# Performance work log

Hardware: AMD Instinct MI355X
Metric: run time of the kernel (lower is better)

Reference implementation:

```python
import jax, jax.numpy as jnp
import numpy as np

B, TV, TL = 4, 13600, 256
VD, LD, E, H = 256, 768, 256, 8
HD = E // H
SCALE = HD ** -0.5
CLAMP = 50000.0
NEG = -9e15


def _xavier(k, out_d, in_d):
    lim = np.sqrt(6.0 / (in_d + out_d)).astype(np.float32)
    return jax.random.uniform(k, (out_d, in_d), minval=-lim, maxval=lim, dtype=jnp.float32)


def setup_inputs() -> dict:
    key = jax.random.key(0)
    ks = jax.random.split(key, 10)
    return {
        "v": jax.random.normal(ks[0], (B, TV, VD), dtype=jnp.float32),
        "l": jax.random.normal(ks[1], (B, TL, LD), dtype=jnp.float32),
        "v_pos": jax.random.normal(ks[2], (B, TV, VD), dtype=jnp.float32),
        "attention_mask_v": jnp.ones((B, TV), dtype=jnp.float32),
        "attention_mask_l": jnp.ones((B, TL), dtype=jnp.float32),
        "Wq": _xavier(ks[3], E, VD), "bq": jnp.zeros((E,), jnp.float32),
        "Wk": _xavier(ks[4], E, LD), "bk": jnp.zeros((E,), jnp.float32),
        "Wvv": _xavier(ks[5], E, VD), "bvv": jnp.zeros((E,), jnp.float32),
        "Wvl": _xavier(ks[6], E, LD), "bvl": jnp.zeros((E,), jnp.float32),
        "Wov": _xavier(ks[7], VD, E), "bov": jnp.zeros((VD,), jnp.float32),
        "Wol": _xavier(ks[8], LD, E), "bol": jnp.zeros((LD,), jnp.float32),
    }


def _heads(x):  # [B, T, E] -> [B, H, T, HD]
    b, t, _ = x.shape
    return x.reshape(b, t, H, HD).transpose(0, 2, 1, 3)


def reference(v, l, v_pos, attention_mask_v, attention_mask_l,
              Wq, bq, Wk, bk, Wvv, bvv, Wvl, bvl, Wov, bov, Wol, bol):
    # projections (eval mode: dropout disabled)
    q = _heads(((v + v_pos) @ Wq.T + bq) * SCALE)        # [B,H,TV,HD]
    k = _heads(l @ Wk.T + bk)                             # [B,H,TL,HD]
    val_v = _heads(v @ Wvv.T + bvv)                       # [B,H,TV,HD]
    val_l = _heads(l @ Wvl.T + bvl)                       # [B,H,TL,HD]

    # shared scores, computed once: [B,H,TV,TL]
    aw = jnp.einsum('bhtd,bhsd->bhts', q, k)
    aw = jnp.clip(aw, -CLAMP, CLAMP)

    # language-direction scores: transpose, stabilize, clamp
    aw_l = aw.transpose(0, 1, 3, 2)                       # [B,H,TL,TV]
    aw_l = aw_l - jnp.max(aw_l, axis=-1, keepdims=True)
    aw_l = jnp.clip(aw_l, -CLAMP, CLAMP)
    # torch masked_fill(mask==0, NEG) then + : nonzero mask values are ADDED
    mv = jnp.where(attention_mask_v == 0, NEG, attention_mask_v)[:, None, None, :]
    aw_l = aw_l + mv
    p_l = jax.nn.softmax(aw_l, axis=-1)

    # vision-direction scores
    ml = jnp.where(attention_mask_l == 0, NEG, attention_mask_l)[:, None, None, :]
    p_v = jax.nn.softmax(aw + ml, axis=-1)

    out_v = jnp.einsum('bhts,bhsd->bhtd', p_v, val_l)     # [B,H,TV,HD]
    out_l = jnp.einsum('bhst,bhtd->bhsd', p_l, val_v)     # [B,H,TL,HD]
    out_v = out_v.transpose(0, 2, 1, 3).reshape(B, TV, E) @ Wov.T + bov
    out_l = out_l.transpose(0, 2, 1, 3).reshape(B, TL, E) @ Wol.T + bol
    return (out_v, out_l)
```

## Files before the change

kernel.cpp:

```cpp
#include <hip/hip_runtime.h>
#include <math.h>


typedef unsigned short u16;
typedef unsigned int   u32;
typedef __attribute__((ext_vector_type(4))) u16 us4;
typedef __attribute__((ext_vector_type(8))) u16 us8;
typedef __attribute__((ext_vector_type(8))) short s8b;
typedef __attribute__((ext_vector_type(4))) float f4;

#define B_   4
#define TV_  13600
#define TL_  256
#define VD_  256
#define LD_  768
#define E_   256
#define H_   8
#define HD_  32
#define PREC 36

static constexpr float SCALE_  = 0.17677669529663687f;
static constexpr float CLAMP_  = 50000.0f;
static constexpr float NEG_    = -9e15f;
static constexpr float LOG2E_  = 1.4426950408889634f;

__device__ __forceinline__ float bf2f(u16 x) {
    return __uint_as_float(((u32)x) << 16);
}
__device__ __forceinline__ u16 f2bf(float f) {
    u32 u = __float_as_uint(f);
    u += 0x7fffu + ((u >> 16) & 1u);
    return (u16)(u >> 16);
}

__device__ __forceinline__ s8b frag32(const u16* base, int row, int q) {
    int slot = q ^ ((row >> 1) & 3);
    return *(const s8b*)(base + row * 32 + slot * 8);
}

__global__ void sniff_kernel(const void* __restrict__ mask, int* __restrict__ flag) {
    if (threadIdx.x == 0 && blockIdx.x == 0) {
        u32 w = *(const u32*)mask;
        *flag = (w == 0x3F800000u) ? 1 : 0;
    }
}

__global__ __launch_bounds__(256) void prep_v_kernel(
    const int* __restrict__ flag, const void* __restrict__ v,
    const void* __restrict__ vp, u16* __restrict__ vb, u16* __restrict__ vqb)
{
    const bool f32 = (*flag != 0);
    const size_t n = (size_t)B_ * TV_ * VD_;
    size_t i = ((size_t)blockIdx.x * 256 + threadIdx.x) * 4;
    const size_t stride = (size_t)gridDim.x * 256 * 4;
    for (; i < n; i += stride) {
        float a[4], b[4];
        if (f32) {
            float4 x = ((const float4*)v)[i >> 2];
            float4 y = ((const float4*)vp)[i >> 2];
            a[0]=x.x; a[1]=x.y; a[2]=x.z; a[3]=x.w;
            b[0]=y.x; b[1]=y.y; b[2]=y.z; b[3]=y.w;
        } else {
            us4 x = ((const us4*)v)[i >> 2];
            us4 y = ((const us4*)vp)[i >> 2];
            #pragma unroll
            for (int j = 0; j < 4; ++j) { a[j]=bf2f(x[j]); b[j]=bf2f(y[j]); }
        }
        us4 o1, o2;
        #pragma unroll
        for (int j = 0; j < 4; ++j) { o1[j]=f2bf(a[j]); o2[j]=f2bf(a[j]+b[j]); }
        ((us4*)vb)[i >> 2] = o1;
        ((us4*)vqb)[i >> 2] = o2;
    }
}

struct Seg { const void* src; void* dst; int n; int toF32; };
struct PrepArgs { Seg s[13]; };

__global__ __launch_bounds__(256) void prep_rest_kernel(
    const int* __restrict__ flag, PrepArgs args)
{
    const bool f32 = (*flag != 0);
    for (int k = 0; k < 13; ++k) {
        Seg sg = args.s[k];
        for (int j = blockIdx.x * 256 + threadIdx.x; j < sg.n;
             j += gridDim.x * 256) {
            float x = f32 ? ((const float*)sg.src)[j] : bf2f(((const u16*)sg.src)[j]);
            if (sg.toF32) ((float*)sg.dst)[j] = x;
            else          ((u16*)sg.dst)[j]   = f2bf(x);
        }
    }
}

template<bool CEXT>
__global__ __launch_bounds__(256) void gemm_mfma(
    const int* __restrict__ flag,
    const u16* __restrict__ A, const u16* __restrict__ W,
    const float* __restrict__ bias, void* __restrict__ C, size_t c_off,
    int N, int K, float scale)
{
    __shared__ __align__(16) u16 As[128 * 32];
    __shared__ __align__(16) u16 Bs[128 * 32];
    const int tid  = threadIdx.x;
    const int lane = tid & 63, wid = tid >> 6;
    const int wm = wid >> 1, wn = wid & 1;
    const size_t m0 = (size_t)blockIdx.x * 128;
    const int n0 = blockIdx.y * 128;

    const int srow = tid >> 1;
    const int half = tid & 1;
    const int ssw  = (srow >> 1) & 3;
    const int sl0  = half * 2, sl1 = half * 2 + 1;

    f4 acc[4][4];
    #pragma unroll
    for (int i = 0; i < 4; ++i)
        #pragma unroll
        for (int j = 0; j < 4; ++j) acc[i][j] = (f4){0.f, 0.f, 0.f, 0.f};

    for (int k0 = 0; k0 < K; k0 += 32) {
        {
            const u16* ga = A + (m0 + srow) * (size_t)K + k0;
            *(us8*)&As[srow*32 + sl0*8] = *(const us8*)(ga + (sl0 ^ ssw) * 8);
            *(us8*)&As[srow*32 + sl1*8] = *(const us8*)(ga + (sl1 ^ ssw) * 8);
            const u16* gb = W + ((size_t)(n0 + srow)) * (size_t)K + k0;
            *(us8*)&Bs[srow*32 + sl0*8] = *(const us8*)(gb + (sl0 ^ ssw) * 8);
            *(us8*)&Bs[srow*32 + sl1*8] = *(const us8*)(gb + (sl1 ^ ssw) * 8);
        }
        __syncthreads();
        s8b af[4], bf[4];
        const int q = lane >> 4;
        #pragma unroll
        for (int mt = 0; mt < 4; ++mt)
            af[mt] = frag32(As, wm*64 + mt*16 + (lane & 15), q);
        #pragma unroll
        for (int nt = 0; nt < 4; ++nt)
            bf[nt] = frag32(Bs, wn*64 + nt*16 + (lane & 15), q);
        #pragma unroll
        for (int mt = 0; mt < 4; ++mt)
            #pragma unroll
            for (int nt = 0; nt < 4; ++nt)
                acc[mt][nt] = __builtin_amdgcn_mfma_f32_16x16x32_bf16(
                    af[mt], bf[nt], acc[mt][nt], 0, 0, 0);
        __syncthreads();
    }

    const int q = lane >> 4;
    const bool f32out = CEXT ? (*flag != 0) : false;
    #pragma unroll
    for (int nt = 0; nt < 4; ++nt) {
        const int col = n0 + wn*64 + nt*16 + (lane & 15);
        const float bv = bias[col];
        #pragma unroll
        for (int mt = 0; mt < 4; ++mt) {
            #pragma unroll
            for (int reg = 0; reg < 4; ++reg) {
                const size_t row = m0 + wm*64 + mt*16 + q*4 + reg;
                const float val = (acc[mt][nt][reg] + bv) * scale;
                const size_t idx = c_off + row * (size_t)N + col;
                if (CEXT && f32out) ((float*)C)[idx] = val;
                else                ((u16*)C)[idx]   = f2bf(val);
            }
        }
    }
}

__global__ __launch_bounds__(256, 4) void attn_v_mfma(
    const int* __restrict__ flag,
    const u16* __restrict__ qm, const u16* __restrict__ km,
    const u16* __restrict__ vm, const void* __restrict__ maskl,
    u16* __restrict__ outm)
{
    __shared__ __align__(16) u16 Qs[64 * 32];
    __shared__ __align__(16) u16 Ks[256 * 32];
    __shared__ __align__(16) u16 VTs[32 * 264];
    __shared__ float mls[256];

    const int tid = threadIdx.x, lane = tid & 63, wid = tid >> 6;
    const int bb = blockIdx.z, hh = blockIdx.y;
    const int t0 = blockIdx.x * 64;
    const int q  = lane >> 4;
    const int l15 = lane & 15;

    {
        int row = tid >> 2, slot = tid & 3;
        int sw = (row >> 1) & 3;
        int tg = t0 + row; if (tg >= TV_) tg = TV_ - 1;
        const u16* gp = qm + ((size_t)(bb*TV_ + tg)) * E_ + hh*HD_;
        *(us8*)&Qs[row*32 + slot*8] = *(const us8*)(gp + ((slot ^ sw) * 8));
    }
    {
        int s = tid, sw = (s >> 1) & 3;
        const u16* gp = km + ((size_t)(bb*TL_ + s)) * E_ + hh*HD_;
        #pragma unroll
        for (int slot = 0; slot < 4; ++slot)
            *(us8*)&Ks[s*32 + slot*8] = *(const us8*)(gp + ((slot ^ sw) * 8));
    }
    {
        int s = tid;
        const u16* gp = vm + ((size_t)(bb*TL_ + s)) * E_ + hh*HD_;
        #pragma unroll
        for (int d0 = 0; d0 < 32; d0 += 8) {
            us8 vv = *(const us8*)(gp + d0);
            #pragma unroll
            for (int j = 0; j < 8; ++j) VTs[(d0 + j)*264 + s] = vv[j];
        }
        float mv = (*flag) ? ((const float*)maskl)[(size_t)bb*TL_ + s]
                           : bf2f(((const u16*)maskl)[(size_t)bb*TL_ + s]);
        mls[s] = (mv == 0.0f) ? NEG_ : mv;
    }
    __syncthreads();

    const s8b qf = frag32(Qs, wid*16 + l15, q);
    f4 sacc[16];
    #pragma unroll
    for (int mt = 0; mt < 16; ++mt) {
        s8b kf = frag32(Ks, mt*16 + l15, q);
        f4 z = {0.f, 0.f, 0.f, 0.f};
        sacc[mt] = __builtin_amdgcn_mfma_f32_16x16x32_bf16(kf, qf, z, 0, 0, 0);
    }

    float vmax = -1e30f;
    #pragma unroll
    for (int mt = 0; mt < 16; ++mt) {
        f4 mv4 = *(const f4*)&mls[mt*16 + q*4];
        #pragma unroll
        for (int r = 0; r < 4; ++r) {
            float v = fminf(fmaxf(sacc[mt][r], -CLAMP_), CLAMP_) + mv4[r];
            sacc[mt][r] = v;
            vmax = fmaxf(vmax, v);
        }
    }
    vmax = fmaxf(vmax, __shfl_xor(vmax, 16));
    vmax = fmaxf(vmax, __shfl_xor(vmax, 32));

    float sum = 0.f;
    us4 pws[16];
    #pragma unroll
    for (int mt = 0; mt < 16; ++mt) {
        #pragma unroll
        for (int r = 0; r < 4; ++r) {
            float p = exp2f((sacc[mt][r] - vmax) * LOG2E_);
            u16 pb = f2bf(p);
            pws[mt][r] = pb;
            sum += bf2f(pb);
        }
    }
    sum += __shfl_xor(sum, 16);
    sum += __shfl_xor(sum, 32);
    float Lreg[4];
    #pragma unroll
    for (int r = 0; r < 4; ++r) Lreg[r] = __shfl(sum, q*4 + r);

    __syncthreads();

    u16* myP = Ks + wid * (16 * 40);
    f4 oacc[2];
    oacc[0] = (f4){0.f,0.f,0.f,0.f};
    oacc[1] = (f4){0.f,0.f,0.f,0.f};
    #pragma unroll
    for (int ks = 0; ks < 8; ++ks) {
        *(us4*)&myP[l15*40 + q*4]      = pws[2*ks];
        *(us4*)&myP[l15*40 + 16 + q*4] = pws[2*ks + 1];
        s8b pa = *(const s8b*)&myP[l15*40 + q*8];
        #pragma unroll
        for (int nt = 0; nt < 2; ++nt) {
            s8b vb = *(const s8b*)&VTs[(nt*16 + l15)*264 + ks*32 + q*8];
            oacc[nt] = __builtin_amdgcn_mfma_f32_16x16x32_bf16(pa, vb, oacc[nt], 0, 0, 0);
        }
    }

    #pragma unroll
    for (int r = 0; r < 4; ++r) {
        const int tg = t0 + wid*16 + q*4 + r;
        if (tg < TV_) {
            const float inv = 1.0f / Lreg[r];
            #pragma unroll
            for (int nt = 0; nt < 2; ++nt)
                outm[((size_t)(bb*TV_ + tg)) * E_ + hh*HD_ + nt*16 + l15] =
                    f2bf(oacc[nt][r] * inv);
        }
    }
}

__global__ __launch_bounds__(256, 6) void attn_l_mfma(
    const int* __restrict__ flag,
    const u16* __restrict__ qm, const u16* __restrict__ km,
    const u16* __restrict__ vm, const void* __restrict__ maskv,
    u16* __restrict__ part, int nchunk, int chunk)
{
    __shared__ __align__(16) u16 smem0[128 * 40];
    __shared__ __align__(16) u16 Qs[32 * 32];
    __shared__ __align__(16) u16 VTs[32 * 32];
    __shared__ float mvs[32];

    const int tid = threadIdx.x, lane = tid & 63, wid = tid >> 6;
    const int bb = blockIdx.z, hh = blockIdx.y;
    const int tc  = blockIdx.x >> 1;
    const int s0b = (blockIdx.x & 1) * 128;
    const int q = lane >> 4;
    const bool f32m = (*flag != 0);

    {
        int row = tid >> 1, half = tid & 1;
        int sw = (row >> 1) & 3;
        const u16* gp = km + ((size_t)(bb*TL_ + s0b + row)) * E_ + hh*HD_;
        int sl0 = half*2, sl1 = half*2 + 1;
        *(us8*)&smem0[row*32 + sl0*8] = *(const us8*)(gp + ((sl0 ^ sw) * 8));
        *(us8*)&smem0[row*32 + sl1*8] = *(const us8*)(gp + ((sl1 ^ sw) * 8));
    }
    s8b bk[2];
    bk[0] = frag32(smem0, wid*32 + (lane & 15), q);
    bk[1] = frag32(smem0, wid*32 + 16 + (lane & 15), q);

    float m_s[2], l_s[2];
    f4 oacc[2][2];
    m_s[0] = m_s[1] = -1e30f;
    l_s[0] = l_s[1] = 0.f;
    oacc[0][0] = oacc[0][1] = oacc[1][0] = oacc[1][1] = (f4){0.f,0.f,0.f,0.f};

    const int nstep = chunk >> 5;
    for (int step = 0; step < nstep; ++step) {
        const int t0 = tc * chunk + step * 32;
        if (tid < 128) {
            int row = tid >> 2, slot = tid & 3;
            int sw = (row >> 1) & 3;
            const u16* gp = qm + ((size_t)(bb*TV_ + t0 + row)) * E_ + hh*HD_;
            *(us8*)&Qs[row*32 + slot*8] = *(const us8*)(gp + ((slot ^ sw) * 8));
        } else {
            int t2 = tid - 128;
            int trow = t2 >> 2, d0 = (t2 & 3) * 8;
            us8 vv = *(const us8*)(vm + ((size_t)(bb*TV_ + t0 + trow)) * E_ + hh*HD_ + d0);
            #pragma unroll
            for (int j = 0; j < 8; ++j) {
                int d = d0 + j;
                VTs[d*32 + (((trow >> 3) ^ ((d >> 1) & 3)) * 8) + (trow & 7)] = vv[j];
            }
        }
        if (tid < 32) {
            float mv = f32m ? ((const float*)maskv)[(size_t)bb*TV_ + t0 + tid]
                            : bf2f(((const u16*)maskv)[(size_t)bb*TV_ + t0 + tid]);
            mvs[tid] = (mv == 0.0f) ? NEG_ : mv;
        }
        __syncthreads();

        s8b aq0 = frag32(Qs, (lane & 15), q);
        s8b aq1 = frag32(Qs, 16 + (lane & 15), q);
        f4 sacc[2][2];
        {
            f4 zz = {0.f, 0.f, 0.f, 0.f};
            sacc[0][0] = __builtin_amdgcn_mfma_f32_16x16x32_bf16(aq0, bk[0], zz, 0, 0, 0);
            sacc[0][1] = __builtin_amdgcn_mfma_f32_16x16x32_bf16(aq0, bk[1], zz, 0, 0, 0);
            sacc[1][0] = __builtin_amdgcn_mfma_f32_16x16x32_bf16(aq1, bk[0], zz, 0, 0, 0);
            sacc[1][1] = __builtin_amdgcn_mfma_f32_16x16x32_bf16(aq1, bk[1], zz, 0, 0, 0);
        }

        float mvq[2][4];
        #pragma unroll
        for (int tt = 0; tt < 2; ++tt)
            #pragma unroll
            for (int r = 0; r < 4; ++r) mvq[tt][r] = mvs[tt*16 + q*4 + r];

        #pragma unroll
        for (int st = 0; st < 2; ++st) {
            float vmax = -1e30f;
            #pragma unroll
            for (int tt = 0; tt < 2; ++tt)
                #pragma unroll
                for (int r = 0; r < 4; ++r) {
                    float v = fminf(fmaxf(sacc[tt][st][r], -CLAMP_), CLAMP_) + mvq[tt][r];
                    sacc[tt][st][r] = v;
                    vmax = fmaxf(vmax, v);
                }
            vmax = fmaxf(vmax, __shfl_xor(vmax, 16));
            vmax = fmaxf(vmax, __shfl_xor(vmax, 32));
            float m = m_s[st];
            if (__any(vmax > m + 8.0f)) {
                float nm = fmaxf(m, vmax);
                float al = exp2f((m - nm) * LOG2E_);
                l_s[st] *= al;
                #pragma unroll
                for (int dt = 0; dt < 2; ++dt)
                    #pragma unroll
                    for (int r = 0; r < 4; ++r) oacc[dt][st][r] *= al;
                m_s[st] = m = nm;
            }
            const int ls = wid*32 + st*16 + (lane & 15);
            float ps = 0.f;
            #pragma unroll
            for (int tt = 0; tt < 2; ++tt) {
                us4 pw;
                #pragma unroll
                for (int r = 0; r < 4; ++r) {
                    u16 pb = f2bf(exp2f((sacc[tt][st][r] - m) * LOG2E_));
                    pw[r] = pb;
                    ps += bf2f(pb);
                }
                *(us4*)&smem0[ls*40 + tt*16 + q*4] = pw;
            }
            ps += __shfl_xor(ps, 16);
            ps += __shfl_xor(ps, 32);
            l_s[st] += ps;
        }

        s8b av0 = frag32(VTs, (lane & 15), q);
        s8b av1 = frag32(VTs, 16 + (lane & 15), q);
        #pragma unroll
        for (int st = 0; st < 2; ++st) {
            s8b bp = *(const s8b*)&smem0[(wid*32 + st*16 + (lane & 15))*40 + q*8];
            oacc[0][st] = __builtin_amdgcn_mfma_f32_16x16x32_bf16(av0, bp, oacc[0][st], 0, 0, 0);
            oacc[1][st] = __builtin_amdgcn_mfma_f32_16x16x32_bf16(av1, bp, oacc[1][st], 0, 0, 0);
        }
        __syncthreads();
    }

    #pragma unroll
    for (int st = 0; st < 2; ++st) {
        const int s = s0b + wid*32 + st*16 + (lane & 15);
        u16* rec = part + ((size_t)((bb*H_ + hh)*TL_ + s) * nchunk + tc) * PREC;
        #pragma unroll
        for (int dt = 0; dt < 2; ++dt)
            #pragma unroll
            for (int r = 0; r < 4; ++r)
                rec[dt*16 + q*4 + r] = f2bf(oacc[dt][st][r]);
        if (q == 0) {
            *(float*)(rec + 32) = m_s[st];
            *(float*)(rec + 34) = l_s[st];
        }
    }
}

__global__ __launch_bounds__(256) void attn_l_merge(
    const u16* __restrict__ part, u16* __restrict__ outm, int nchunk)
{
    const int R = blockIdx.x * 8 + (threadIdx.x >> 5);
    const int d = threadIdx.x & 31;
    const u16* rec0 = part + (size_t)R * nchunk * PREC;
    float m = -1e30f;
    for (int c = 0; c < nchunk; ++c)
        m = fmaxf(m, *(const float*)(rec0 + c*PREC + 32));
    float L = 0.f, o = 0.f;
    for (int c = 0; c < nchunk; ++c) {
        float mc = *(const float*)(rec0 + c*PREC + 32);
        float lc = *(const float*)(rec0 + c*PREC + 34);
        float w  = exp2f((mc - m) * LOG2E_);
        L += lc * w;
        o += bf2f(rec0[c*PREC + d]) * w;
    }
    o /= L;
    const int bb = R >> 11, hh = (R >> 8) & 7, ss = R & 255;
    outm[(size_t)(bb*TL_ + ss) * E_ + hh*HD_ + d] = f2bf(o);
}

extern "C" void kernel_launch(void* const* d_in, const int* in_sizes, int n_in,
                              void* d_out, int out_size, void* d_ws, size_t ws_size,
                              hipStream_t stream)
{
    const void* v     = d_in[0];
    const void* l     = d_in[1];
    const void* vpos  = d_in[2];
    const void* maskv = d_in[3];
    const void* maskl = d_in[4];
    const void* Wq  = d_in[5];   const void* bq  = d_in[6];
    const void* Wk  = d_in[7];   const void* bk  = d_in[8];
    const void* Wvv = d_in[9];   const void* bvv = d_in[10];
    const void* Wvl = d_in[11];  const void* bvl = d_in[12];
    const void* Wov = d_in[13];  const void* bov = d_in[14];
    const void* Wol = d_in[15];  const void* bol = d_in[16];

    const size_t BIG   = (size_t)B_*TV_*E_*2;
    const size_t TLBUF = (size_t)B_*TL_*E_*2;
    const size_t LBUF  = (size_t)B_*TL_*LD_*2;
    auto part_bytes = [](int nc) { return (size_t)B_*H_*TL_ * (size_t)nc * (PREC*2); };

    const size_t fixed = 512 + 2*(BIG+256) + (LBUF+256) + 3*(TLBUF+256)
                       + (131072+256)*3 + (393216+256)*3 + (8192+256);
    const int cand[3] = {25, 17, 5};
    int nchunk = 5;
    for (int i = 0; i < 3; ++i)
        if (fixed + part_bytes(cand[i]) + 256 <= ws_size) { nchunk = cand[i]; break; }
    const int chunk = TV_ / nchunk;

    char* ws = (char*)d_ws;
    size_t off = 0;
    auto carve = [&](size_t bytes) -> char* {
        char* p = ws + off;
        off += (bytes + 255) & ~(size_t)255;
        return p;
    };
    int*   flag    = (int*)carve(512);
    u16*   slot1   = (u16*)carve(BIG);
    u16*   slot2   = (u16*)carve(BIG);
    u16*   lb      = (u16*)carve(LBUF);
    u16*   k_ws    = (u16*)carve(TLBUF);
    u16*   vall_ws = (u16*)carve(TLBUF);
    u16*   attnl_ws= (u16*)carve(TLBUF);
    u16*   wqb     = (u16*)carve(131072);
    u16*   wkb     = (u16*)carve(393216);
    u16*   wvvb    = (u16*)carve(131072);
    u16*   wvlb    = (u16*)carve(393216);
    u16*   wovb    = (u16*)carve(131072);
    u16*   wolb    = (u16*)carve(393216);
    float* biasf   = (float*)carve(8192);
    u16*   part_ws = (u16*)carve(part_bytes(nchunk));

    u16* vb    = slot1;
    u16* vqb   = slot2;
    u16* valv  = slot2;
    u16* attnv = slot1;
    u16* q_ws  = (u16*)d_out;

    float* bqf  = biasf;        float* bkf  = biasf + 256;
    float* bvvf = biasf + 512;  float* bvlf = biasf + 768;
    float* bovf = biasf + 1024; float* bolf = biasf + 1280;

    const dim3 blk(256);
    const size_t outl_off = (size_t)B_*TV_*VD_;

    sniff_kernel<<<1, 64, 0, stream>>>(maskv, flag);

    prep_v_kernel<<<2048, blk, 0, stream>>>(flag, v, vpos, vb, vqb);
    PrepArgs pa;
    pa.s[0]  = { l,   lb,   B_*TL_*LD_, 0 };
    pa.s[1]  = { Wq,  wqb,  E_*VD_,     0 };
    pa.s[2]  = { Wk,  wkb,  E_*LD_,     0 };
    pa.s[3]  = { Wvv, wvvb, E_*VD_,     0 };
    pa.s[4]  = { Wvl, wvlb, E_*LD_,     0 };
    pa.s[5]  = { Wov, wovb, VD_*E_,     0 };
    pa.s[6]  = { Wol, wolb, LD_*E_,     0 };
    pa.s[7]  = { bq,  bqf,  E_,  1 };
    pa.s[8]  = { bk,  bkf,  E_,  1 };
    pa.s[9]  = { bvv, bvvf, E_,  1 };
    pa.s[10] = { bvl, bvlf, E_,  1 };
    pa.s[11] = { bov, bovf, VD_, 1 };
    pa.s[12] = { bol, bolf, LD_, 1 };
    prep_rest_kernel<<<256, blk, 0, stream>>>(flag, pa);

    gemm_mfma<false><<<dim3(425, 2), blk, 0, stream>>>(flag, vqb, wqb,  bqf,  q_ws,    0, E_, VD_, SCALE_);
    gemm_mfma<false><<<dim3(425, 2), blk, 0, stream>>>(flag, vb,  wvvb, bvvf, valv,    0, E_, VD_, 1.0f);
    gemm_mfma<false><<<dim3(8,   2), blk, 0, stream>>>(flag, lb,  wkb,  bkf,  k_ws,    0, E_, LD_, 1.0f);
    gemm_mfma<false><<<dim3(8,   2), blk, 0, stream>>>(flag, lb,  wvlb, bvlf, vall_ws, 0, E_, LD_, 1.0f);

    attn_l_mfma <<<dim3(nchunk*2, H_, B_), blk, 0, stream>>>(flag, q_ws, k_ws, valv, maskv, part_ws, nchunk, chunk);
    attn_l_merge<<<dim3(B_*H_*TL_/8),      blk, 0, stream>>>(part_ws, attnl_ws, nchunk);
    attn_v_mfma <<<dim3((TV_+63)/64, H_, B_), blk, 0, stream>>>(flag, q_ws, k_ws, vall_ws, maskl, attnv);

    gemm_mfma<true><<<dim3(425, 2), blk, 0, stream>>>(flag, attnv,    wovb, bovf, d_out, 0,        VD_, E_, 1.0f);
    gemm_mfma<true><<<dim3(8,   6), blk, 0, stream>>>(flag, attnl_ws, wolb, bolf, d_out, outl_off, LD_, E_, 1.0f);
}
```

Measured before the change: 488.9 us.

## Double-buffer Q/V/mask tiles in attn_l and raise wave priority around MFMA blocks

The language-direction attention kernel now keeps two shared-memory buffers for the Q tile, transposed V tile and mask values. The next step's global loads are issued into registers before the current step's MFMAs and written to the alternate buffer afterwards, which leaves one barrier per step and lets global latency overlap compute. s_setprio(1)/(0) brackets are also added around the MFMA sections in the GEMM, vision attention and language attention kernels to favour waves issuing matrix ops. Both changes cost extra registers and LDS, which could reduce occupancy at the launch bound of 6.

Measured after the change: 485.8 us. About the same (-0.6%).

```diff
diff --git a/kernel.cpp b/kernel.cpp
--- a/kernel.cpp
+++ b/kernel.cpp
@@ -136,12 +136,14 @@
         #pragma unroll
         for (int nt = 0; nt < 4; ++nt)
             bf[nt] = frag32(Bs, wn*64 + nt*16 + (lane & 15), q);
+        __builtin_amdgcn_s_setprio(1);
         #pragma unroll
         for (int mt = 0; mt < 4; ++mt)
             #pragma unroll
             for (int nt = 0; nt < 4; ++nt)
                 acc[mt][nt] = __builtin_amdgcn_mfma_f32_16x16x32_bf16(
                     af[mt], bf[nt], acc[mt][nt], 0, 0, 0);
+        __builtin_amdgcn_s_setprio(0);
         __syncthreads();
     }
 
@@ -213,12 +215,14 @@
 
     const s8b qf = frag32(Qs, wid*16 + l15, q);
     f4 sacc[16];
+    __builtin_amdgcn_s_setprio(1);
     #pragma unroll
     for (int mt = 0; mt < 16; ++mt) {
         s8b kf = frag32(Ks, mt*16 + l15, q);
         f4 z = {0.f, 0.f, 0.f, 0.f};
         sacc[mt] = __builtin_amdgcn_mfma_f32_16x16x32_bf16(kf, qf, z, 0, 0, 0);
     }
+    __builtin_amdgcn_s_setprio(0);
 
     float vmax = -1e30f;
     #pragma unroll
@@ -258,6 +262,7 @@
     f4 oacc[2];
     oacc[0] = (f4){0.f,0.f,0.f,0.f};
     oacc[1] = (f4){0.f,0.f,0.f,0.f};
+    __builtin_amdgcn_s_setprio(1);
     #pragma unroll
     for (int ks = 0; ks < 8; ++ks) {
         *(us4*)&myP[l15*40 + q*4]      = pws[2*ks];
@@ -269,6 +274,7 @@
             oacc[nt] = __builtin_amdgcn_mfma_f32_16x16x32_bf16(pa, vb, oacc[nt], 0, 0, 0);
         }
     }
+    __builtin_amdgcn_s_setprio(0);
 
     #pragma unroll
     for (int r = 0; r < 4; ++r) {
@@ -290,15 +296,15 @@
     u16* __restrict__ part, int nchunk, int chunk)
 {
     __shared__ __align__(16) u16 smem0[128 * 40];
-    __shared__ __align__(16) u16 Qs[32 * 32];
-    __shared__ __align__(16) u16 VTs[32 * 32];
-    __shared__ float mvs[32];
+    __shared__ __align__(16) u16 Qd[2][32 * 32];
+    __shared__ __align__(16) u16 Vd[2][32 * 32];
+    __shared__ float mvd[2][32];
 
     const int tid = threadIdx.x, lane = tid & 63, wid = tid >> 6;
     const int bb = blockIdx.z, hh = blockIdx.y;
     const int tc  = blockIdx.x >> 1;
     const int s0b = (blockIdx.x & 1) * 128;
-    const int q = lane >> 4;
+    const int q = lane >> 4, l15 = lane & 15;
     const bool f32m = (*flag != 0);
 
     {
@@ -309,9 +315,12 @@
         *(us8*)&smem0[row*32 + sl0*8] = *(const us8*)(gp + ((sl0 ^ sw) * 8));
         *(us8*)&smem0[row*32 + sl1*8] = *(const us8*)(gp + ((sl1 ^ sw) * 8));
     }
-    s8b bk[2];
-    bk[0] = frag32(smem0, wid*32 + (lane & 15), q);
-    bk[1] = frag32(smem0, wid*32 + 16 + (lane & 15), q);
+    s8b bk0 = frag32(smem0, wid*32 + l15, q);
+    s8b bk1 = frag32(smem0, wid*32 + 16 + l15, q);
+
+    const int qrow = tid >> 2, qslot = tid & 3;
+    const int qsw  = (qrow >> 1) & 3;
+    const int vrow = (tid - 128) >> 2, vd0 = (tid & 3) * 8;
 
     float m_s[2], l_s[2];
     f4 oacc[2][2];
@@ -319,47 +328,71 @@
     l_s[0] = l_s[1] = 0.f;
     oacc[0][0] = oacc[0][1] = oacc[1][0] = oacc[1][1] = (f4){0.f,0.f,0.f,0.f};
 
+    {
+        const int t0 = tc * chunk;
+        if (tid < 128) {
+            us8 qreg = *(const us8*)(qm + ((size_t)(bb*TV_ + t0 + qrow)) * E_
+                                     + hh*HD_ + ((qslot ^ qsw) * 8));
+            *(us8*)&Qd[0][qrow*32 + qslot*8] = qreg;
+            if (tid < 32) {
+                float mv = f32m ? ((const float*)maskv)[(size_t)bb*TV_ + t0 + tid]
+                                : bf2f(((const u16*)maskv)[(size_t)bb*TV_ + t0 + tid]);
+                mvd[0][tid] = (mv == 0.0f) ? NEG_ : mv;
+            }
+        } else {
+            us8 vreg = *(const us8*)(vm + ((size_t)(bb*TV_ + t0 + vrow)) * E_
+                                     + hh*HD_ + vd0);
+            #pragma unroll
+            for (int j = 0; j < 8; ++j) {
+                int d = vd0 + j;
+                Vd[0][d*32 + (((vrow >> 3) ^ ((d >> 1) & 3)) * 8) + (vrow & 7)] = vreg[j];
+            }
+        }
+    }
+    __syncthreads();
+
     const int nstep = chunk >> 5;
     for (int step = 0; step < nstep; ++step) {
-        const int t0 = tc * chunk + step * 32;
-        if (tid < 128) {
-            int row = tid >> 2, slot = tid & 3;
-            int sw = (row >> 1) & 3;
-            const u16* gp = qm + ((size_t)(bb*TV_ + t0 + row)) * E_ + hh*HD_;
-            *(us8*)&Qs[row*32 + slot*8] = *(const us8*)(gp + ((slot ^ sw) * 8));
-        } else {
-            int t2 = tid - 128;
-            int trow = t2 >> 2, d0 = (t2 & 3) * 8;
-            us8 vv = *(const us8*)(vm + ((size_t)(bb*TV_ + t0 + trow)) * E_ + hh*HD_ + d0);
-            #pragma unroll
-            for (int j = 0; j < 8; ++j) {
-                int d = d0 + j;
-                VTs[d*32 + (((trow >> 3) ^ ((d >> 1) & 3)) * 8) + (trow & 7)] = vv[j];
-            }
-        }
-        if (tid < 32) {
-            float mv = f32m ? ((const float*)maskv)[(size_t)bb*TV_ + t0 + tid]
-                            : bf2f(((const u16*)maskv)[(size_t)bb*TV_ + t0 + tid]);
-            mvs[tid] = (mv == 0.0f) ? NEG_ : mv;
-        }
-        __syncthreads();
-
-        s8b aq0 = frag32(Qs, (lane & 15), q);
-        s8b aq1 = frag32(Qs, 16 + (lane & 15), q);
+        const int cur = step & 1;
+        const u16* Qc = Qd[cur];
+        const u16* Vc = Vd[cur];
+        const float* mc = mvd[cur];
+
+        us8 qreg, vreg;
+        float mreg = 0.f;
+        const bool pf = (step + 1 < nstep);
+        if (pf) {
+            const int t1 = tc * chunk + (step + 1) * 32;
+            if (tid < 128) {
+                qreg = *(const us8*)(qm + ((size_t)(bb*TV_ + t1 + qrow)) * E_
+                                     + hh*HD_ + ((qslot ^ qsw) * 8));
+                if (tid < 32)
+                    mreg = f32m ? ((const float*)maskv)[(size_t)bb*TV_ + t1 + tid]
+                                : bf2f(((const u16*)maskv)[(size_t)bb*TV_ + t1 + tid]);
+            } else {
+                vreg = *(const us8*)(vm + ((size_t)(bb*TV_ + t1 + vrow)) * E_
+                                     + hh*HD_ + vd0);
+            }
+        }
+
+        s8b aq0 = frag32(Qc, l15, q);
+        s8b aq1 = frag32(Qc, 16 + l15, q);
         f4 sacc[2][2];
+        __builtin_amdgcn_s_setprio(1);
         {
             f4 zz = {0.f, 0.f, 0.f, 0.f};
-            sacc[0][0] = __builtin_amdgcn_mfma_f32_16x16x32_bf16(aq0, bk[0], zz, 0, 0, 0);
-            sacc[0][1] = __builtin_amdgcn_mfma_f32_16x16x32_bf16(aq0, bk[1], zz, 0, 0, 0);
-            sacc[1][0] = __builtin_amdgcn_mfma_f32_16x16x32_bf16(aq1, bk[0], zz, 0, 0, 0);
-            sacc[1][1] = __builtin_amdgcn_mfma_f32_16x16x32_bf16(aq1, bk[1], zz, 0, 0, 0);
-        }
+            sacc[0][0] = __builtin_amdgcn_mfma_f32_16x16x32_bf16(aq0, bk0, zz, 0, 0, 0);
+            sacc[0][1] = __builtin_amdgcn_mfma_f32_16x16x32_bf16(aq0, bk1, zz, 0, 0, 0);
+            sacc[1][0] = __builtin_amdgcn_mfma_f32_16x16x32_bf16(aq1, bk0, zz, 0, 0, 0);
+            sacc[1][1] = __builtin_amdgcn_mfma_f32_16x16x32_bf16(aq1, bk1, zz, 0, 0, 0);
+        }
+        __builtin_amdgcn_s_setprio(0);
 
         float mvq[2][4];
         #pragma unroll
         for (int tt = 0; tt < 2; ++tt)
             #pragma unroll
-            for (int r = 0; r < 4; ++r) mvq[tt][r] = mvs[tt*16 + q*4 + r];
+            for (int r = 0; r < 4; ++r) mvq[tt][r] = mc[tt*16 + q*4 + r];
 
         #pragma unroll
         for (int st = 0; st < 2; ++st) {
@@ -385,7 +418,7 @@
                     for (int r = 0; r < 4; ++r) oacc[dt][st][r] *= al;
                 m_s[st] = m = nm;
             }
-            const int ls = wid*32 + st*16 + (lane & 15);
+            const int ls = wid*32 + st*16 + l15;
             float ps = 0.f;
             #pragma unroll
             for (int tt = 0; tt < 2; ++tt) {
@@ -403,20 +436,35 @@
             l_s[st] += ps;
         }
 
-        s8b av0 = frag32(VTs, (lane & 15), q);
-        s8b av1 = frag32(VTs, 16 + (lane & 15), q);
+        s8b av0 = frag32(Vc, l15, q);
+        s8b av1 = frag32(Vc, 16 + l15, q);
+        __builtin_amdgcn_s_setprio(1);
         #pragma unroll
         for (int st = 0; st < 2; ++st) {
-            s8b bp = *(const s8b*)&smem0[(wid*32 + st*16 + (lane & 15))*40 + q*8];
+            s8b bp = *(const s8b*)&smem0[(wid*32 + st*16 + l15)*40 + q*8];
             oacc[0][st] = __builtin_amdgcn_mfma_f32_16x16x32_bf16(av0, bp, oacc[0][st], 0, 0, 0);
             oacc[1][st] = __builtin_amdgcn_mfma_f32_16x16x32_bf16(av1, bp, oacc[1][st], 0, 0, 0);
         }
+        __builtin_amdgcn_s_setprio(0);
+
+        if (pf) {
+            if (tid < 128) {
+                *(us8*)&Qd[cur ^ 1][qrow*32 + qslot*8] = qreg;
+                if (tid < 32) mvd[cur ^ 1][tid] = (mreg == 0.0f) ? NEG_ : mreg;
+            } else {
+                #pragma unroll
+                for (int j = 0; j < 8; ++j) {
+                    int d = vd0 + j;
+                    Vd[cur ^ 1][d*32 + (((vrow >> 3) ^ ((d >> 1) & 3)) * 8) + (vrow & 7)] = vreg[j];
+                }
+            }
+        }
         __syncthreads();
     }
 
     #pragma unroll
     for (int st = 0; st < 2; ++st) {
-        const int s = s0b + wid*32 + st*16 + (lane & 15);
+        const int s = s0b + wid*32 + st*16 + l15;
         u16* rec = part + ((size_t)((bb*H_ + hh)*TL_ + s) * nchunk + tc) * PREC;
         #pragma unroll
         for (int dt = 0; dt < 2; ++dt)
```
